# Performance work log

Measured on AMD Instinct MI355X. Metric: run time of the kernel, lower is better.

Reference implementation:

```python
import jax, jax.numpy as jnp
import numpy as np

B, M, IN_DIM = 8, 2048, 512
N_HEAD, ATTN_DIM = 8, 64
HEAD_DIM = N_HEAD * ATTN_DIM  # 512
SCALE = HEAD_DIM ** (-0.5)


def setup_inputs() -> dict:
    key = jax.random.key(0)
    ks = jax.random.split(key, 5)
    s = IN_DIM ** -0.5
    return {
        "x": jax.random.normal(ks[0], (B, M, IN_DIM), dtype=jnp.float32),
        "Wq": jax.random.normal(ks[1], (IN_DIM, HEAD_DIM), dtype=jnp.float32) * s,
        "Wk": jax.random.normal(ks[2], (IN_DIM, HEAD_DIM), dtype=jnp.float32) * s,
        "Wv": jax.random.normal(ks[3], (IN_DIM, HEAD_DIM), dtype=jnp.float32) * s,
        "Wo": jax.random.normal(ks[4], (HEAD_DIM, IN_DIM), dtype=jnp.float32) * s,
        "bo": jnp.zeros((IN_DIM,), dtype=jnp.float32),
    }


def _split_heads(t):
    # [B, M, H*D] -> [B, H, M, D]
    b, m, _ = t.shape
    return t.reshape(b, m, N_HEAD, ATTN_DIM).transpose(0, 2, 1, 3)


def reference(x, Wq, Wk, Wv, Wo, bo):
    q = _split_heads(x @ Wq)  # bhmd
    k = _split_heads(x @ Wk)
    v = _split_heads(x @ Wv)
    # Faithful to source: logits DIVIDED by scale=head_dim**-0.5 (i.e. * sqrt(head_dim))
    logits = jnp.einsum('bhid,bhjd->bhij', q, k) / SCALE
    scores = jax.nn.softmax(logits, axis=-1)
    weighted = jnp.einsum('bhij,bhjd->bhid', scores, v)  # [B,H,M,D]
    merged = weighted.transpose(0, 2, 1, 3).reshape(x.shape[0], x.shape[1], HEAD_DIM)
    return merged @ Wo + bo
```

## Files before the change

kernel.cpp:

```cpp
#include <hip/hip_runtime.h>
#include <hip/hip_bf16.h>
#include <cstdint>

#define DI __device__ __forceinline__

typedef __attribute__((ext_vector_type(8))) short bf16x8;
typedef __attribute__((ext_vector_type(4))) short s16x4;
typedef __attribute__((ext_vector_type(4))) float f32x4;
typedef __attribute__((ext_vector_type(2))) int   i32x2;

static constexpr int BATCH = 8, SEQ = 2048;
static constexpr int ROWS = BATCH * SEQ;
static constexpr float SCALE_Q = (float)(22.627416997969522 * 1.4426950408889634);

DI short f2bf(float f) { __hip_bfloat16 h = __float2bfloat16(f); return *reinterpret_cast<short*>(&h); }
DI float bf2f(short s) { __hip_bfloat16 h; *reinterpret_cast<short*>(&h) = s; return __bfloat162float(h); }
DI unsigned pack2(float a, float b) {
  return (unsigned)(unsigned short)f2bf(a) | ((unsigned)(unsigned short)f2bf(b) << 16);
}

DI void gload_lds16(const void* gp, void* lp) {
  __builtin_amdgcn_global_load_lds(
      (__attribute__((address_space(1))) void*)const_cast<void*>(gp),
      (__attribute__((address_space(3))) void*)lp, 16, 0, 0);
}
DI f32x4 mfma16(bf16x8 a, bf16x8 b, f32x4 c) {
  return __builtin_amdgcn_mfma_f32_16x16x32_bf16(a, b, c, 0, 0, 0);
}

__global__ __launch_bounds__(256)
void prep_w(const float* __restrict__ Wq, const float* __restrict__ Wk,
            const float* __restrict__ Wv, const float* __restrict__ Wo,
            short* __restrict__ Wqk_hi, short* __restrict__ Wqk_lo,
            short* __restrict__ Wv_t, short* __restrict__ Wo_t)
{
  __shared__ float t[64][65];
  const int blk = blockIdx.x;
  const int mat = blk >> 6;
  const int tile = blk & 63;
  const int tn = (tile & 7) * 64;
  const int tk = (tile >> 3) * 64;
  const float* src = mat == 0 ? Wq : mat == 1 ? Wk : mat == 2 ? Wv : Wo;
  const float scale = (mat == 0) ? SCALE_Q : 1.0f;
  const int tid = threadIdx.x;
#pragma unroll
  for (int i = 0; i < 16; ++i) {
    int idx = i * 256 + tid;
    t[idx >> 6][idx & 63] = src[(size_t)(tk + (idx >> 6)) * 512 + tn + (idx & 63)];
  }
  __syncthreads();
#pragma unroll
  for (int i = 0; i < 16; ++i) {
    int idx = i * 256 + tid;
    int nn = idx >> 6, kk = idx & 63;
    float v = t[kk][nn] * scale;
    short hb = f2bf(v);
    size_t o = (size_t)(tn + nn) * 512 + (tk + kk);
    if (mat <= 1) {
      Wqk_hi[(size_t)mat * 512 * 512 + o] = hb;
      Wqk_lo[(size_t)mat * 512 * 512 + o] = f2bf(v - bf2f(hb));
    } else if (mat == 2) Wv_t[o] = hb;
    else Wo_t[o] = hb;
  }
}

template<int MODE>
__global__ __launch_bounds__(256, 2)
void gemm_kern(const float* __restrict__ Axf, const short* __restrict__ Axb,
               const short* __restrict__ Bhg, const short* __restrict__ Blg,
               short* __restrict__ O0h, short* __restrict__ O0l,
               short* __restrict__ O1h, short* __restrict__ O1l,
               float* __restrict__ Of, const float* __restrict__ bias)
{
  constexpr bool SPLIT = (MODE == 0);
  __shared__ __align__(16) short Ah[128 * 32];
  __shared__ __align__(16) short Bh[128 * 32];
  __shared__ __align__(16) short Al[SPLIT ? 128 * 32 : 16];
  __shared__ __align__(16) short Bl[SPLIT ? 128 * 32 : 16];

  const int tid = threadIdx.x;
  const int wave = tid >> 6, lane = tid & 63, lo = lane & 15, hi4 = lane >> 4;
  const int wr = wave >> 1, wc = wave & 1;
  const int m0 = blockIdx.y * 128, n0 = blockIdx.x * 128;

  f32x4 acc[4][4] = {};

  for (int kt = 0; kt < 16; ++kt) {
    __syncthreads();
    if constexpr (MODE != 2) {
#pragma unroll
      for (int r2 = 0; r2 < 4; ++r2) {
        int idx = r2 * 256 + tid;
        int row = idx >> 3, c4 = idx & 7;
        const float4 v = *reinterpret_cast<const float4*>(Axf + (size_t)(m0 + row) * 512 + kt * 32 + c4 * 4);
        s16x4 h4, l4;
#pragma unroll
        for (int j = 0; j < 4; ++j) {
          float f = ((const float*)&v)[j];
          short hb = f2bf(f);
          h4[j] = hb;
          if constexpr (SPLIT) l4[j] = f2bf(f - bf2f(hb));
        }
        int off = row * 64 + ((((c4 >> 1) ^ ((row >> 1) & 3)) << 4) | ((c4 & 1) << 3));
        *reinterpret_cast<s16x4*>((char*)Ah + off) = h4;
        if constexpr (SPLIT) *reinterpret_cast<s16x4*>((char*)Al + off) = l4;
      }
    } else {
#pragma unroll
      for (int is = 0; is < 2; ++is) {
        int rowl = is * 64 + wave * 16 + (lane >> 2);
        int chunk = (lane & 3) ^ ((rowl >> 1) & 3);
        const char* src = (const char*)Axb + ((size_t)(m0 + rowl) * 512 + kt * 32) * 2 + chunk * 16;
        gload_lds16(src, (char*)Ah + is * 4096 + wave * 1024);
      }
    }
#pragma unroll
    for (int is = 0; is < 2; ++is) {
      int rowl = is * 64 + wave * 16 + (lane >> 2);
      int chunk = (lane & 3) ^ ((rowl >> 1) & 3);
      size_t gb = ((size_t)(n0 + rowl) * 512 + kt * 32) * 2 + chunk * 16;
      gload_lds16((const char*)Bhg + gb, (char*)Bh + is * 4096 + wave * 1024);
      if constexpr (SPLIT)
        gload_lds16((const char*)Blg + gb, (char*)Bl + is * 4096 + wave * 1024);
    }
    __syncthreads();
    bf16x8 a_h[4], a_l[4], b_h[4], b_l[4];
#pragma unroll
    for (int m = 0; m < 4; ++m) {
      int ar = wr * 64 + m * 16 + lo;
      int off = ar * 64 + ((hi4 ^ ((ar >> 1) & 3)) << 4);
      a_h[m] = *reinterpret_cast<const bf16x8*>((const char*)Ah + off);
      if constexpr (SPLIT) a_l[m] = *reinterpret_cast<const bf16x8*>((const char*)Al + off);
    }
#pragma unroll
    for (int n = 0; n < 4; ++n) {
      int br = wc * 64 + n * 16 + lo;
      int off = br * 64 + ((hi4 ^ ((br >> 1) & 3)) << 4);
      b_h[n] = *reinterpret_cast<const bf16x8*>((const char*)Bh + off);
      if constexpr (SPLIT) b_l[n] = *reinterpret_cast<const bf16x8*>((const char*)Bl + off);
    }
#pragma unroll
    for (int m = 0; m < 4; ++m)
#pragma unroll
      for (int n = 0; n < 4; ++n) {
        acc[m][n] = mfma16(a_h[m], b_h[n], acc[m][n]);
        if constexpr (SPLIT) {
          acc[m][n] = mfma16(a_h[m], b_l[n], acc[m][n]);
          acc[m][n] = mfma16(a_l[m], b_h[n], acc[m][n]);
        }
      }
  }
#pragma unroll
  for (int m = 0; m < 4; ++m)
#pragma unroll
    for (int n = 0; n < 4; ++n) {
      if constexpr (MODE == 1) {
        int cg = n0 + wc * 64 + n * 16 + lo;
        int rgb = m0 + wr * 64 + m * 16 + hi4 * 4;
        int bh = (rgb >> 11) * 8 + (cg >> 6);
        s16x4 vt4;
#pragma unroll
        for (int j = 0; j < 4; ++j) vt4[j] = f2bf(acc[m][n][j]);
        size_t o = ((size_t)(bh * 64 + (cg & 63))) * 2048 + (rgb & 2047);
        *reinterpret_cast<s16x4*>(O0h + o) = vt4;
      } else {
#pragma unroll
        for (int j = 0; j < 4; ++j) {
          int rg = m0 + wr * 64 + m * 16 + hi4 * 4 + j;
          int cg = n0 + wc * 64 + n * 16 + lo;
          float v = acc[m][n][j];
          if constexpr (MODE == 2) {
            Of[(size_t)rg * 512 + cg] = v + bias[cg];
          } else {
            int mat = cg >> 9;
            int c9 = cg & 511;
            size_t o = ((size_t)((rg >> 11) * 8 + (c9 >> 6)) * 2048 + (rg & 2047)) * 64 + (c9 & 63);
            short hb = f2bf(v);
            short lb = f2bf(v - bf2f(hb));
            if (mat == 0) { O0h[o] = hb; O0l[o] = lb; }
            else          { O1h[o] = hb; O1l[o] = lb; }
          }
        }
      }
    }
}

__global__ __launch_bounds__(256, 2)
void attn_kern(const short* __restrict__ Qh, const short* __restrict__ Ql,
               const short* __restrict__ Kh, const short* __restrict__ Kl,
               const short* __restrict__ VTg, short* __restrict__ Og)
{
  __shared__ __align__(16) short Ksh[64 * 64];
  __shared__ __align__(16) short Ksl[64 * 64];
  __shared__ __align__(16) short Vts[64 * 64];
  __shared__ __align__(16) short Ps[4][1024];

  const int bh = blockIdx.y, qt = blockIdx.x;
  const int tid = threadIdx.x, wave = tid >> 6, lane = tid & 63, lo = lane & 15, hi4 = lane >> 4;
  const int q0 = qt * 64;

  const size_t qoff = ((size_t)bh * 2048 + q0 + wave * 16 + lo) * 64;
  bf16x8 qh[2], ql[2];
#pragma unroll
  for (int kk = 0; kk < 2; ++kk) {
    qh[kk] = *reinterpret_cast<const bf16x8*>(Qh + qoff + kk * 32 + hi4 * 8);
    ql[kk] = *reinterpret_cast<const bf16x8*>(Ql + qoff + kk * 32 + hi4 * 8);
  }

  f32x4 acc_o[4] = {};
  float m_run = -3.0e38f, l_run = 0.f;

  short* pw = &Ps[wave][0];

  for (int kt = 0; kt < 32; ++kt) {
    __syncthreads();
#pragma unroll
    for (int is = 0; is < 2; ++is) {
      int rowl = is * 32 + wave * 8 + (lane >> 3);
      int chunk = (lane & 7) ^ (rowl & 7);
      size_t gbK = ((size_t)bh * 2048 + kt * 64 + rowl) * 128 + chunk * 16;
      gload_lds16((const char*)Kh + gbK, (char*)Ksh + is * 4096 + wave * 1024);
      gload_lds16((const char*)Kl + gbK, (char*)Ksl + is * 4096 + wave * 1024);
      size_t gbV = (((size_t)bh * 64 + rowl) * 2048 + kt * 64) * 2 + chunk * 16;
      gload_lds16((const char*)VTg + gbV, (char*)Vts + is * 4096 + wave * 1024);
    }
    __syncthreads();

    f32x4 s[4];
    __builtin_amdgcn_s_setprio(1);
#pragma unroll
    for (int kb = 0; kb < 4; ++kb) {
      f32x4 t = {0.f, 0.f, 0.f, 0.f};
#pragma unroll
      for (int kk = 0; kk < 2; ++kk) {
        int krow = kb * 16 + lo;
        int off = krow * 128 + ((kk * 64 + hi4 * 16) ^ ((krow & 7) << 4));
        bf16x8 kh8 = *reinterpret_cast<const bf16x8*>((const char*)Ksh + off);
        bf16x8 kl8 = *reinterpret_cast<const bf16x8*>((const char*)Ksl + off);
        t = mfma16(kh8, qh[kk], t);
        t = mfma16(kl8, qh[kk], t);
        t = mfma16(kh8, ql[kk], t);
      }
      s[kb] = t;
    }
    __builtin_amdgcn_s_setprio(0);

    float mt = s[0][0];
#pragma unroll
    for (int kb = 0; kb < 4; ++kb)
#pragma unroll
      for (int j = 0; j < 4; ++j) mt = fmaxf(mt, s[kb][j]);
    mt = fmaxf(mt, __shfl_xor(mt, 16));
    mt = fmaxf(mt, __shfl_xor(mt, 32));
    if (!__all(mt - m_run <= 8.0f)) {
      float mn = fmaxf(m_run, mt);
      float corr = exp2f(m_run - mn);
      m_run = mn;
      l_run *= corr;
#pragma unroll
      for (int j = 0; j < 4; ++j) {
        float cj = __shfl(corr, hi4 * 4 + j);
#pragma unroll
        for (int db = 0; db < 4; ++db) acc_o[db][j] *= cj;
      }
    }
    float ls = 0.f;
#pragma unroll
    for (int kb = 0; kb < 4; ++kb)
#pragma unroll
      for (int j = 0; j < 4; ++j) {
        float p = exp2f(s[kb][j] - m_run);
        s[kb][j] = p;
        ls += p;
      }
    ls += __shfl_xor(ls, 16);
    ls += __shfl_xor(ls, 32);
    l_run += ls;

#pragma unroll
    for (int kb = 0; kb < 4; ++kb) {
      i32x2 w;
      w.x = (int)pack2(s[kb][0], s[kb][1]);
      w.y = (int)pack2(s[kb][2], s[kb][3]);
      int off = lo * 128 + ((kb * 32 + hi4 * 8) ^ ((lo & 7) << 4));
      *reinterpret_cast<i32x2*>((char*)pw + off) = w;
    }
    __builtin_amdgcn_sched_barrier(0);
    bf16x8 pa[2];
#pragma unroll
    for (int kk = 0; kk < 2; ++kk) {
      int off = lo * 128 + ((kk * 64 + hi4 * 16) ^ ((lo & 7) << 4));
      pa[kk] = *reinterpret_cast<const bf16x8*>((const char*)pw + off);
    }

    __builtin_amdgcn_s_setprio(1);
#pragma unroll
    for (int db = 0; db < 4; ++db) {
#pragma unroll
      for (int kk = 0; kk < 2; ++kk) {
        int vrow = db * 16 + lo;
        int voff = vrow * 128 + ((kk * 64 + hi4 * 16) ^ ((lo & 7) << 4));
        bf16x8 v8 = *reinterpret_cast<const bf16x8*>((const char*)Vts + voff);
        acc_o[db] = mfma16(pa[kk], v8, acc_o[db]);
      }
    }
    __builtin_amdgcn_s_setprio(0);
  }

  const int b = bh >> 3, h = bh & 7;
#pragma unroll
  for (int j = 0; j < 4; ++j) {
    float lr = __shfl(l_run, hi4 * 4 + j);
    float inv = 1.0f / lr;
    int mrow = q0 + wave * 16 + hi4 * 4 + j;
    size_t base = ((size_t)(b * 2048 + mrow)) * 512 + h * 64;
#pragma unroll
    for (int db = 0; db < 4; ++db)
      Og[base + db * 16 + lo] = f2bf(acc_o[db][j] * inv);
  }
}

extern "C" void kernel_launch(void* const* d_in, const int* in_sizes, int n_in,
                              void* d_out, int out_size, void* d_ws, size_t ws_size,
                              hipStream_t stream) {
  const float* x  = (const float*)d_in[0];
  const float* Wq = (const float*)d_in[1];
  const float* Wk = (const float*)d_in[2];
  const float* Wv = (const float*)d_in[3];
  const float* Wo = (const float*)d_in[4];
  const float* bo = (const float*)d_in[5];
  float* out = (float*)d_out;

  char* ws = (char*)d_ws;
  short* Wqk_hi = (short*)(ws);
  short* Wqk_lo = (short*)(ws + (1 << 20));
  short* Wv_t   = (short*)(ws + (2 << 20));
  short* Wo_t   = (short*)(ws + (2 << 20) + 512 * 512 * 2);
  char* big = ws + 3 * (1 << 20);
  const size_t SZ = (size_t)ROWS * 512 * 2;
  short* Qh = (short*)(big);
  short* Ql = (short*)(big + SZ);
  short* Kh = (short*)(big + 2 * SZ);
  short* Kl = (short*)(big + 3 * SZ);
  short* VT = (short*)(big + 4 * SZ);
  short* Ob = (short*)(big + 5 * SZ);
  (void)in_sizes; (void)n_in; (void)out_size; (void)ws_size;

  prep_w<<<dim3(256), dim3(256), 0, stream>>>(Wq, Wk, Wv, Wo, Wqk_hi, Wqk_lo, Wv_t, Wo_t);
  gemm_kern<0><<<dim3(8, 128), dim3(256), 0, stream>>>(x, nullptr, Wqk_hi, Wqk_lo,
                                                       Qh, Ql, Kh, Kl, nullptr, nullptr);
  gemm_kern<1><<<dim3(4, 128), dim3(256), 0, stream>>>(x, nullptr, Wv_t, nullptr,
                                                       VT, nullptr, nullptr, nullptr, nullptr, nullptr);
  attn_kern<<<dim3(32, 64), dim3(256), 0, stream>>>(Qh, Ql, Kh, Kl, VT, Ob);
  gemm_kern<2><<<dim3(4, 128), dim3(256), 0, stream>>>(nullptr, Ob, Wo_t, nullptr,
                                                       nullptr, nullptr, nullptr, nullptr, out, bo);
}
```

Before: 402.2 us.

## Pre-split x to bf16 once, double-buffer attention K/V tiles, raise MFMA priority

Adds a prep_x kernel that converts x to bf16 hi/lo pairs once. The QK and V projection GEMMs then stage A through direct global-to-LDS loads instead of converting fp32 in every tile. The attention kernel double-buffers its K and V tiles, issuing the next tile's loads before computing the current one so memory overlaps with MFMA work, and uses one barrier per iteration. The GEMM also raises wave priority around its MFMA block. Costs are an extra kernel launch, extra workspace traffic for x (xh aliases the Ob buffer), and doubled attention LDS, which may lower occupancy.

```diff
diff --git a/kernel.cpp b/kernel.cpp
--- a/kernel.cpp
+++ b/kernel.cpp
@@ -26,6 +26,27 @@
 }
 DI f32x4 mfma16(bf16x8 a, bf16x8 b, f32x4 c) {
   return __builtin_amdgcn_mfma_f32_16x16x32_bf16(a, b, c, 0, 0, 0);
+}
+
+__global__ __launch_bounds__(256)
+void prep_x(const float* __restrict__ x, short* __restrict__ xh, short* __restrict__ xl)
+{
+  const int g0 = blockIdx.x * 1024 + threadIdx.x;
+#pragma unroll
+  for (int i = 0; i < 4; ++i) {
+    int g = g0 + i * 256;
+    const float4 v = *reinterpret_cast<const float4*>(x + (size_t)g * 4);
+    s16x4 h4, l4;
+#pragma unroll
+    for (int j = 0; j < 4; ++j) {
+      float f = ((const float*)&v)[j];
+      short hb = f2bf(f);
+      h4[j] = hb;
+      l4[j] = f2bf(f - bf2f(hb));
+    }
+    *reinterpret_cast<s16x4*>(xh + (size_t)g * 4) = h4;
+    *reinterpret_cast<s16x4*>(xl + (size_t)g * 4) = l4;
+  }
 }
 
 __global__ __launch_bounds__(256)
@@ -66,7 +87,7 @@
 
 template<int MODE>
 __global__ __launch_bounds__(256, 2)
-void gemm_kern(const float* __restrict__ Axf, const short* __restrict__ Axb,
+void gemm_kern(const short* __restrict__ Axh, const short* __restrict__ Axl,
                const short* __restrict__ Bhg, const short* __restrict__ Blg,
                short* __restrict__ O0h, short* __restrict__ O0l,
                short* __restrict__ O1h, short* __restrict__ O1l,
@@ -87,37 +108,14 @@
 
   for (int kt = 0; kt < 16; ++kt) {
     __syncthreads();
-    if constexpr (MODE != 2) {
-#pragma unroll
-      for (int r2 = 0; r2 < 4; ++r2) {
-        int idx = r2 * 256 + tid;
-        int row = idx >> 3, c4 = idx & 7;
-        const float4 v = *reinterpret_cast<const float4*>(Axf + (size_t)(m0 + row) * 512 + kt * 32 + c4 * 4);
-        s16x4 h4, l4;
-#pragma unroll
-        for (int j = 0; j < 4; ++j) {
-          float f = ((const float*)&v)[j];
-          short hb = f2bf(f);
-          h4[j] = hb;
-          if constexpr (SPLIT) l4[j] = f2bf(f - bf2f(hb));
-        }
-        int off = row * 64 + ((((c4 >> 1) ^ ((row >> 1) & 3)) << 4) | ((c4 & 1) << 3));
-        *reinterpret_cast<s16x4*>((char*)Ah + off) = h4;
-        if constexpr (SPLIT) *reinterpret_cast<s16x4*>((char*)Al + off) = l4;
-      }
-    } else {
-#pragma unroll
-      for (int is = 0; is < 2; ++is) {
-        int rowl = is * 64 + wave * 16 + (lane >> 2);
-        int chunk = (lane & 3) ^ ((rowl >> 1) & 3);
-        const char* src = (const char*)Axb + ((size_t)(m0 + rowl) * 512 + kt * 32) * 2 + chunk * 16;
-        gload_lds16(src, (char*)Ah + is * 4096 + wave * 1024);
-      }
-    }
 #pragma unroll
     for (int is = 0; is < 2; ++is) {
       int rowl = is * 64 + wave * 16 + (lane >> 2);
       int chunk = (lane & 3) ^ ((rowl >> 1) & 3);
+      size_t ab = ((size_t)(m0 + rowl) * 512 + kt * 32) * 2 + chunk * 16;
+      gload_lds16((const char*)Axh + ab, (char*)Ah + is * 4096 + wave * 1024);
+      if constexpr (SPLIT)
+        gload_lds16((const char*)Axl + ab, (char*)Al + is * 4096 + wave * 1024);
       size_t gb = ((size_t)(n0 + rowl) * 512 + kt * 32) * 2 + chunk * 16;
       gload_lds16((const char*)Bhg + gb, (char*)Bh + is * 4096 + wave * 1024);
       if constexpr (SPLIT)
@@ -139,6 +137,7 @@
       b_h[n] = *reinterpret_cast<const bf16x8*>((const char*)Bh + off);
       if constexpr (SPLIT) b_l[n] = *reinterpret_cast<const bf16x8*>((const char*)Bl + off);
     }
+    __builtin_amdgcn_s_setprio(1);
 #pragma unroll
     for (int m = 0; m < 4; ++m)
 #pragma unroll
@@ -149,6 +148,7 @@
           acc[m][n] = mfma16(a_l[m], b_h[n], acc[m][n]);
         }
       }
+    __builtin_amdgcn_s_setprio(0);
   }
 #pragma unroll
   for (int m = 0; m < 4; ++m)
@@ -190,9 +190,9 @@
                const short* __restrict__ Kh, const short* __restrict__ Kl,
                const short* __restrict__ VTg, short* __restrict__ Og)
 {
-  __shared__ __align__(16) short Ksh[64 * 64];
-  __shared__ __align__(16) short Ksl[64 * 64];
-  __shared__ __align__(16) short Vts[64 * 64];
+  __shared__ __align__(16) short Ksh[2][64 * 64];
+  __shared__ __align__(16) short Ksl[2][64 * 64];
+  __shared__ __align__(16) short Vts[2][64 * 64];
   __shared__ __align__(16) short Ps[4][1024];
 
   const int bh = blockIdx.y, qt = blockIdx.x;
@@ -212,19 +212,25 @@
 
   short* pw = &Ps[wave][0];
 
-  for (int kt = 0; kt < 32; ++kt) {
-    __syncthreads();
+  auto STAGE = [&](int kt, int buf) {
 #pragma unroll
     for (int is = 0; is < 2; ++is) {
       int rowl = is * 32 + wave * 8 + (lane >> 3);
       int chunk = (lane & 7) ^ (rowl & 7);
       size_t gbK = ((size_t)bh * 2048 + kt * 64 + rowl) * 128 + chunk * 16;
-      gload_lds16((const char*)Kh + gbK, (char*)Ksh + is * 4096 + wave * 1024);
-      gload_lds16((const char*)Kl + gbK, (char*)Ksl + is * 4096 + wave * 1024);
+      gload_lds16((const char*)Kh + gbK, (char*)&Ksh[buf][0] + is * 4096 + wave * 1024);
+      gload_lds16((const char*)Kl + gbK, (char*)&Ksl[buf][0] + is * 4096 + wave * 1024);
       size_t gbV = (((size_t)bh * 64 + rowl) * 2048 + kt * 64) * 2 + chunk * 16;
-      gload_lds16((const char*)VTg + gbV, (char*)Vts + is * 4096 + wave * 1024);
-    }
-    __syncthreads();
+      gload_lds16((const char*)VTg + gbV, (char*)&Vts[buf][0] + is * 4096 + wave * 1024);
+    }
+  };
+
+  STAGE(0, 0);
+  __syncthreads();
+
+  for (int kt = 0; kt < 32; ++kt) {
+    const int cur = kt & 1;
+    if (kt < 31) STAGE(kt + 1, cur ^ 1);
 
     f32x4 s[4];
     __builtin_amdgcn_s_setprio(1);
@@ -235,8 +241,8 @@
       for (int kk = 0; kk < 2; ++kk) {
         int krow = kb * 16 + lo;
         int off = krow * 128 + ((kk * 64 + hi4 * 16) ^ ((krow & 7) << 4));
-        bf16x8 kh8 = *reinterpret_cast<const bf16x8*>((const char*)Ksh + off);
-        bf16x8 kl8 = *reinterpret_cast<const bf16x8*>((const char*)Ksl + off);
+        bf16x8 kh8 = *reinterpret_cast<const bf16x8*>((const char*)&Ksh[cur][0] + off);
+        bf16x8 kl8 = *reinterpret_cast<const bf16x8*>((const char*)&Ksl[cur][0] + off);
         t = mfma16(kh8, qh[kk], t);
         t = mfma16(kl8, qh[kk], t);
         t = mfma16(kh8, ql[kk], t);
@@ -300,11 +306,13 @@
       for (int kk = 0; kk < 2; ++kk) {
         int vrow = db * 16 + lo;
         int voff = vrow * 128 + ((kk * 64 + hi4 * 16) ^ ((lo & 7) << 4));
-        bf16x8 v8 = *reinterpret_cast<const bf16x8*>((const char*)Vts + voff);
+        bf16x8 v8 = *reinterpret_cast<const bf16x8*>((const char*)&Vts[cur][0] + voff);
         acc_o[db] = mfma16(pa[kk], v8, acc_o[db]);
       }
     }
     __builtin_amdgcn_s_setprio(0);
+
+    __syncthreads();
   }
 
   const int b = bh >> 3, h = bh & 7;
@@ -344,14 +352,17 @@
   short* Kl = (short*)(big + 3 * SZ);
   short* VT = (short*)(big + 4 * SZ);
   short* Ob = (short*)(big + 5 * SZ);
+  short* xh = Ob;
+  short* xl = (short*)(big + 6 * SZ);
   (void)in_sizes; (void)n_in; (void)out_size; (void)ws_size;
 
   prep_w<<<dim3(256), dim3(256), 0, stream>>>(Wq, Wk, Wv, Wo, Wqk_hi, Wqk_lo, Wv_t, Wo_t);
-  gemm_kern<0><<<dim3(8, 128), dim3(256), 0, stream>>>(x, nullptr, Wqk_hi, Wqk_lo,
+  prep_x<<<dim3(2048), dim3(256), 0, stream>>>(x, xh, xl);
+  gemm_kern<0><<<dim3(8, 128), dim3(256), 0, stream>>>(xh, xl, Wqk_hi, Wqk_lo,
                                                        Qh, Ql, Kh, Kl, nullptr, nullptr);
-  gemm_kern<1><<<dim3(4, 128), dim3(256), 0, stream>>>(x, nullptr, Wv_t, nullptr,
+  gemm_kern<1><<<dim3(4, 128), dim3(256), 0, stream>>>(xh, nullptr, Wv_t, nullptr,
                                                        VT, nullptr, nullptr, nullptr, nullptr, nullptr);
   attn_kern<<<dim3(32, 64), dim3(256), 0, stream>>>(Qh, Ql, Kh, Kl, VT, Ob);
-  gemm_kern<2><<<dim3(4, 128), dim3(256), 0, stream>>>(nullptr, Ob, Wo_t, nullptr,
+  gemm_kern<2><<<dim3(4, 128), dim3(256), 0, stream>>>(Ob, nullptr, Wo_t, nullptr,
                                                        nullptr, nullptr, nullptr, nullptr, out, bo);
 }
```

New measurement: 429.1 us. 6.7% more time.
